# Optimization experiments

Measured on AMD Instinct MI355X. Metric: run time of the kernel, lower is better.

## Reference

```python
import jax, jax.numpy as jnp
import numpy as np

B, BITS, HID = 4096, 64, 512
EPS = 1e-5
TEMPERATURE = 1.0  # buffer default


def _w(k, shape):
    return jax.random.normal(k, shape, jnp.float32) * 0.02


def setup_inputs() -> dict:
    key = jax.random.key(0)
    ks = jax.random.split(key, 8)
    return {
        "a_bits": jax.random.uniform(ks[0], (B, BITS), jnp.float32),
        "shift_bits": jax.random.uniform(ks[1], (B, BITS), jnp.float32),
        # shift_decoder params
        "W1": _w(ks[2], (HID, BITS)), "b1": jnp.zeros((HID,), jnp.float32),
        "g1": jnp.ones((HID,), jnp.float32), "be1": jnp.zeros((HID,), jnp.float32),
        "W2": _w(ks[3], (HID, HID)), "b2": jnp.zeros((HID,), jnp.float32),
        "g2": jnp.ones((HID,), jnp.float32), "be2": jnp.zeros((HID,), jnp.float32),
        "W3": _w(ks[4], (BITS, HID)), "b3": jnp.zeros((BITS,), jnp.float32),
        # index_net params (input dim = 2*BITS)
        "Wi1": _w(ks[5], (HID, 2 * BITS)), "bi1": jnp.zeros((HID,), jnp.float32),
        "Wi2": _w(ks[6], (HID, HID)), "bi2": jnp.zeros((HID,), jnp.float32),
        "Wi3": _w(ks[7], (BITS, HID)), "bi3": jnp.zeros((BITS,), jnp.float32),
    }


def _layernorm(x, g, b):
    m = jnp.mean(x, axis=-1, keepdims=True)
    v = jnp.mean(jnp.square(x - m), axis=-1, keepdims=True)
    return (x - m) * jax.lax.rsqrt(v + EPS) * g + b


def reference(a_bits, shift_bits, W1, b1, g1, be1, W2, b2, g2, be2, W3, b3,
              Wi1, bi1, Wi2, bi2, Wi3, bi3):
    # shift decoder: Linear -> LN -> ReLU -> Linear -> LN -> ReLU -> Linear
    h = jax.nn.relu(_layernorm(shift_bits @ W1.T + b1, g1, be1))
    h = jax.nn.relu(_layernorm(h @ W2.T + b2, g2, be2))
    shift_logits = h @ W3.T + b3                        # [B, BITS]
    shift_soft = jax.nn.softmax(shift_logits / TEMPERATURE, axis=-1)

    # index_net, vectorized over the output-position loop.
    # combined = [one_hot(i), shift_soft]; the one-hot part of the first Linear
    # just selects column i of Wi1[:, :BITS], so we add it as a [BITS, HID] bias.
    pos_part = Wi1[:, :BITS].T                          # [BITS, HID]
    shift_part = shift_soft @ Wi1[:, BITS:].T           # [B, HID]
    h1 = jax.nn.relu(pos_part[None, :, :] + shift_part[:, None, :] + bi1)  # [B, BITS, HID]
    h2 = jax.nn.relu(jnp.einsum('bph,kh->bpk', h1, Wi2) + bi2)             # [B, BITS, HID]
    idx_logits = jnp.einsum('bph,kh->bpk', h2, Wi3) + bi3                  # [B, BITS, BITS]
    idx_soft = jax.nn.softmax(idx_logits / TEMPERATURE, axis=-1)

    # softmax-weighted gather-sum over a_bits
    return jnp.einsum('bpj,bj->bp', idx_soft, a_bits)   # [B, BITS]
```

## Files before the change

### kernel.cpp

```cpp
#include <hip/hip_runtime.h>
#include <hip/hip_bf16.h>
#include <math.h>

#define B_N 4096
#define BITSN 64
#define HID 512
#define EPSV 1e-5f
#define BT 16

typedef unsigned short ushort_t;
typedef __attribute__((ext_vector_type(8))) short bf16x8;
typedef __attribute__((ext_vector_type(4))) float f32x4;
typedef __attribute__((ext_vector_type(16))) float f32x16;

__device__ __forceinline__ ushort_t f2bf(float f) {
  unsigned u = __float_as_uint(f);
  u += 0x7FFF + ((u >> 16) & 1);
  return (ushort_t)(u >> 16);
}

__device__ __forceinline__ unsigned pack2bf(float lo, float hi) {
  union { __hip_bfloat162 h; unsigned u; } cv;
  cv.h = __float22bfloat162_rn(make_float2(lo, hi));
  return cv.u;
}

__device__ __forceinline__ float bf2f(short v) {
  return __uint_as_float(((unsigned)(unsigned short)v) << 16);
}

__global__ __launch_bounds__(256) void prep_kernel(
    const float* __restrict__ Wi2, const float* __restrict__ Wi3,
    const float* __restrict__ Wi1, const float* __restrict__ W1,
    const float* __restrict__ W2, const float* __restrict__ W3,
    ushort_t* __restrict__ Wi1posTb, ushort_t* __restrict__ W1b,
    ushort_t* __restrict__ W2f, ushort_t* __restrict__ W3b,
    ushort_t* __restrict__ Wi1sb, ushort_t* __restrict__ Wi2f32,
    ushort_t* __restrict__ Wi3g) {
  int idx = blockIdx.x * 256 + threadIdx.x;
  if (idx < 512 * 512) {
    {
      int j = idx & 7, lane = (idx >> 3) & 63;
      int ct = (idx >> 9) & 31, ks = idx >> 14;
      int c = ct * 16 + (lane & 15);
      int k = ks * 32 + (lane >> 4) * 8 + j;
      W2f[idx] = f2bf(W2[c * 512 + k]);
    }
    {
      int j = idx & 7, lane = (idx >> 3) & 63;
      int ct = (idx >> 9) & 15, ks = idx >> 13;
      int c = ct * 32 + (lane & 31);
      int k = ks * 16 + (lane >> 5) * 8 + j;
      Wi2f32[idx] = f2bf(Wi2[c * 512 + k]);
    }
  }
  if (idx < 64 * 512) {
    W3b[idx] = f2bf(W3[idx]);
    int p = idx >> 9, i = idx & 511;
    Wi1posTb[idx] = f2bf(Wi1[i * 128 + p]);
    int e = idx & 7, lane = (idx >> 3) & 63;
    int jt = (idx >> 9) & 1, h = (idx >> 10) & 1;
    int mc = (idx >> 11) & 1, w = idx >> 12;
    int jr = jt * 32 + (lane & 31);
    int c = w * 64 + mc * 32 + 16 * h + 4 * (lane >> 5) + (e & 3) + 8 * (e >> 2);
    Wi3g[idx] = f2bf(Wi3[jr * 512 + c]);
  }
  if (idx < 512 * 64) {
    W1b[idx] = f2bf(W1[idx]);
    int j = idx >> 6, k = idx & 63;
    Wi1sb[idx] = f2bf(Wi1[j * 128 + 64 + k]);
  }
}

__global__ __launch_bounds__(256) void shift2_kernel(
    const float* __restrict__ shift_bits,
    const ushort_t* __restrict__ W1b, const float* __restrict__ b1,
    const float* __restrict__ g1, const float* __restrict__ be1,
    const ushort_t* __restrict__ W2f, const float* __restrict__ b2,
    const float* __restrict__ g2, const float* __restrict__ be2,
    const ushort_t* __restrict__ W3b, const float* __restrict__ b3,
    const ushort_t* __restrict__ Wi1sb, const float* __restrict__ bi1,
    float* __restrict__ sp) {
  __shared__ __align__(16) ushort_t hA[BT * 512];
  __shared__ __align__(16) char reg2[32 * 1024];
  __shared__ float b1s[512], g1s[512], be1s[512];
  __shared__ float b2s[512], g2s[512], be2s[512], bi1s[512];
  __shared__ float red[4][BT][2];
  __shared__ float b3s[64];

  ushort_t* sbt = (ushort_t*)reg2;
  ushort_t* h2  = (ushort_t*)reg2;
  float (*lg32)[68] = (float(*)[68])(reg2 + 16 * 1024);
  ushort_t* sb2 = (ushort_t*)(reg2 + 16 * 1024 + 16 * 68 * 4);

  int b0 = blockIdx.x * BT;
  int t = threadIdx.x, w = t >> 6, l = t & 63, lg = l >> 4, l15 = l & 15;

  b1s[t] = b1[t];  b1s[t + 256] = b1[t + 256];
  g1s[t] = g1[t];  g1s[t + 256] = g1[t + 256];
  be1s[t] = be1[t]; be1s[t + 256] = be1[t + 256];
  b2s[t] = b2[t];  b2s[t + 256] = b2[t + 256];
  g2s[t] = g2[t];  g2s[t + 256] = g2[t + 256];
  be2s[t] = be2[t]; be2s[t + 256] = be2[t + 256];
  bi1s[t] = bi1[t]; bi1s[t + 256] = bi1[t + 256];
  if (t < 64) b3s[t] = b3[t];
  if (t < 128) {
    int row = t >> 3, g = t & 7;
    const float* src = shift_bits + (size_t)(b0 + row) * 64 + g * 8;
    uint4 pk;
    pk.x = (unsigned)f2bf(src[0]) | ((unsigned)f2bf(src[1]) << 16);
    pk.y = (unsigned)f2bf(src[2]) | ((unsigned)f2bf(src[3]) << 16);
    pk.z = (unsigned)f2bf(src[4]) | ((unsigned)f2bf(src[5]) << 16);
    pk.w = (unsigned)f2bf(src[6]) | ((unsigned)f2bf(src[7]) << 16);
    *(uint4*)((char*)sbt + ((row * 128 + g * 16) ^ ((row & 7) << 4))) = pk;
  }
  __syncthreads();

  f32x4 acc[8];
#pragma unroll
  for (int nt = 0; nt < 8; ++nt) acc[nt] = (f32x4){0.f, 0.f, 0.f, 0.f};
#pragma unroll
  for (int ks = 0; ks < 2; ++ks) {
    bf16x8 af = *(const bf16x8*)((char*)sbt + ((l15 * 128 + ks * 64 + lg * 16) ^ ((l15 & 7) << 4)));
#pragma unroll
    for (int nt = 0; nt < 8; ++nt) {
      int c = w * 128 + nt * 16 + l15;
      bf16x8 bfr = *(const bf16x8*)(W1b + (size_t)c * 64 + ks * 32 + lg * 8);
      acc[nt] = __builtin_amdgcn_mfma_f32_16x16x32_bf16(af, bfr, acc[nt], 0, 0, 0);
    }
  }
  {
    float s[4] = {0.f, 0.f, 0.f, 0.f}, q[4] = {0.f, 0.f, 0.f, 0.f};
#pragma unroll
    for (int nt = 0; nt < 8; ++nt) {
      int c = w * 128 + nt * 16 + l15;
      float bb = b1s[c];
#pragma unroll
      for (int r = 0; r < 4; ++r) {
        float x = acc[nt][r] + bb;
        acc[nt][r] = x;
        s[r] += x; q[r] += x * x;
      }
    }
#pragma unroll
    for (int m = 8; m >= 1; m >>= 1)
#pragma unroll
      for (int r = 0; r < 4; ++r) { s[r] += __shfl_xor(s[r], m); q[r] += __shfl_xor(q[r], m); }
    if (l15 == 0)
#pragma unroll
      for (int r = 0; r < 4; ++r) { red[w][4 * lg + r][0] = s[r]; red[w][4 * lg + r][1] = q[r]; }
    __syncthreads();
    float mean[4], rs[4];
#pragma unroll
    for (int r = 0; r < 4; ++r) {
      int p = 4 * lg + r;
      float S = red[0][p][0] + red[1][p][0] + red[2][p][0] + red[3][p][0];
      float Q = red[0][p][1] + red[1][p][1] + red[2][p][1] + red[3][p][1];
      mean[r] = S * (1.0f / 512.0f);
      float var = Q * (1.0f / 512.0f) - mean[r] * mean[r];
      rs[r] = rsqrtf(var + EPSV);
    }
#pragma unroll
    for (int nt = 0; nt < 8; ++nt) {
      int c = w * 128 + nt * 16 + l15;
      float gg = g1s[c], bb = be1s[c];
#pragma unroll
      for (int r = 0; r < 4; ++r) {
        int p = 4 * lg + r;
        float v = (acc[nt][r] - mean[r]) * rs[r] * gg + bb;
        v = v > 0.f ? v : 0.f;
        *(ushort_t*)((char*)hA + ((p * 1024 + c * 2) ^ ((p & 7) << 4))) = f2bf(v);
      }
    }
  }
  __syncthreads();

#pragma unroll
  for (int nt = 0; nt < 8; ++nt) acc[nt] = (f32x4){0.f, 0.f, 0.f, 0.f};
  {
    const bf16x8* w2base = (const bf16x8*)W2f + ((size_t)(w * 8) * 64 + l);
#pragma unroll 2
    for (int step = 0; step < 16; ++step) {
      bf16x8 af = *(const bf16x8*)((char*)hA + ((l15 * 1024 + step * 64 + lg * 16) ^ ((l15 & 7) << 4)));
#pragma unroll
      for (int nt = 0; nt < 8; ++nt) {
        bf16x8 bfr = w2base[((size_t)step * 32 + nt) * 64];
        acc[nt] = __builtin_amdgcn_mfma_f32_16x16x32_bf16(af, bfr, acc[nt], 0, 0, 0);
      }
    }
  }
  __syncthreads();
  {
    float s[4] = {0.f, 0.f, 0.f, 0.f}, q[4] = {0.f, 0.f, 0.f, 0.f};
#pragma unroll
    for (int nt = 0; nt < 8; ++nt) {
      int c = w * 128 + nt * 16 + l15;
      float bb = b2s[c];
#pragma unroll
      for (int r = 0; r < 4; ++r) {
        float x = acc[nt][r] + bb;
        acc[nt][r] = x;
        s[r] += x; q[r] += x * x;
      }
    }
#pragma unroll
    for (int m = 8; m >= 1; m >>= 1)
#pragma unroll
      for (int r = 0; r < 4; ++r) { s[r] += __shfl_xor(s[r], m); q[r] += __shfl_xor(q[r], m); }
    if (l15 == 0)
#pragma unroll
      for (int r = 0; r < 4; ++r) { red[w][4 * lg + r][0] = s[r]; red[w][4 * lg + r][1] = q[r]; }
    __syncthreads();
    float mean[4], rs[4];
#pragma unroll
    for (int r = 0; r < 4; ++r) {
      int p = 4 * lg + r;
      float S = red[0][p][0] + red[1][p][0] + red[2][p][0] + red[3][p][0];
      float Q = red[0][p][1] + red[1][p][1] + red[2][p][1] + red[3][p][1];
      mean[r] = S * (1.0f / 512.0f);
      float var = Q * (1.0f / 512.0f) - mean[r] * mean[r];
      rs[r] = rsqrtf(var + EPSV);
    }
#pragma unroll
    for (int nt = 0; nt < 8; ++nt) {
      int c = w * 128 + nt * 16 + l15;
      float gg = g2s[c], bb = be2s[c];
#pragma unroll
      for (int r = 0; r < 4; ++r) {
        int p = 4 * lg + r;
        float v = (acc[nt][r] - mean[r]) * rs[r] * gg + bb;
        v = v > 0.f ? v : 0.f;
        *(ushort_t*)((char*)h2 + ((p * 1024 + c * 2) ^ ((p & 7) << 4))) = f2bf(v);
      }
    }
  }
  __syncthreads();

  {
    f32x4 a3 = (f32x4){0.f, 0.f, 0.f, 0.f};
#pragma unroll
    for (int ks = 0; ks < 16; ++ks) {
      bf16x8 af = *(const bf16x8*)((char*)h2 + ((l15 * 1024 + ks * 64 + lg * 16) ^ ((l15 & 7) << 4)));
      bf16x8 bfr = *(const bf16x8*)(W3b + (size_t)(w * 16 + l15) * 512 + ks * 32 + lg * 8);
      a3 = __builtin_amdgcn_mfma_f32_16x16x32_bf16(af, bfr, a3, 0, 0, 0);
    }
    int c = w * 16 + l15;
    float bb = b3s[c];
#pragma unroll
    for (int r = 0; r < 4; ++r) lg32[4 * lg + r][c] = a3[r] + bb;
  }
  __syncthreads();

  {
    int r = t >> 4, j = t & 15;
    float v[4];
    float m = -1e30f;
#pragma unroll
    for (int mq = 0; mq < 4; ++mq) { v[mq] = lg32[r][mq * 16 + j]; m = fmaxf(m, v[mq]); }
#pragma unroll
    for (int mk = 8; mk >= 1; mk >>= 1) m = fmaxf(m, __shfl_xor(m, mk));
    float ssum = 0.f;
#pragma unroll
    for (int mq = 0; mq < 4; ++mq) { v[mq] = expf(v[mq] - m); ssum += v[mq]; }
#pragma unroll
    for (int mk = 8; mk >= 1; mk >>= 1) ssum += __shfl_xor(ssum, mk);
    float inv = 1.f / ssum;
#pragma unroll
    for (int mq = 0; mq < 4; ++mq) {
      int c = mq * 16 + j;
      *(ushort_t*)((char*)sb2 + ((r * 128 + c * 2) ^ ((r & 7) << 4))) = f2bf(v[mq] * inv);
    }
  }
  __syncthreads();

  {
    f32x4 a4[8];
#pragma unroll
    for (int nt = 0; nt < 8; ++nt) a4[nt] = (f32x4){0.f, 0.f, 0.f, 0.f};
#pragma unroll
    for (int ks = 0; ks < 2; ++ks) {
      bf16x8 af = *(const bf16x8*)((char*)sb2 + ((l15 * 128 + ks * 64 + lg * 16) ^ ((l15 & 7) << 4)));
#pragma unroll
      for (int nt = 0; nt < 8; ++nt) {
        int c = w * 128 + nt * 16 + l15;
        bf16x8 bfr = *(const bf16x8*)(Wi1sb + (size_t)c * 64 + ks * 32 + lg * 8);
        a4[nt] = __builtin_amdgcn_mfma_f32_16x16x32_bf16(af, bfr, a4[nt], 0, 0, 0);
      }
    }
#pragma unroll
    for (int nt = 0; nt < 8; ++nt) {
      int c = w * 128 + nt * 16 + l15;
      float bb = bi1s[c];
#pragma unroll
      for (int r = 0; r < 4; ++r)
        sp[(size_t)(b0 + 4 * lg + r) * 512 + c] = a4[nt][r] + bb;
    }
  }
}

__global__ __launch_bounds__(512, 4) void big9_kernel(
    const float* __restrict__ a_bits, const float* __restrict__ sp,
    const ushort_t* __restrict__ posTb,
    const ushort_t* __restrict__ Wi2f32, const ushort_t* __restrict__ Wi3g,
    const float* __restrict__ bi2, const float* __restrict__ bi3,
    float* __restrict__ out) {
  __shared__ __align__(16) ushort_t h1s[64 * 512];
  __shared__ float bi2s[512];
  __shared__ float ab[64];
  __shared__ float bi3s[64];

  int b = blockIdx.x, t = threadIdx.x;
  int w = t >> 6, l = t & 63;
  int l31 = l & 31, hi = l >> 5;

  bi2s[t] = bi2[t];
  if (t < 64) { ab[t] = a_bits[b * 64 + t]; bi3s[t] = bi3[t]; }

  {
    const float* sprow = sp + (size_t)b * 512 + l * 8;
    float4 s0 = *(const float4*)(sprow);
    float4 s1 = *(const float4*)(sprow + 4);
#pragma unroll
    for (int g = 0; g < 8; ++g) {
      int p = g * 8 + w;
      bf16x8 pr = *(const bf16x8*)(posTb + (size_t)p * 512 + l * 8);
      float v0 = fmaxf(s0.x + bf2f(pr[0]), 0.f), v1 = fmaxf(s0.y + bf2f(pr[1]), 0.f);
      float v2 = fmaxf(s0.z + bf2f(pr[2]), 0.f), v3 = fmaxf(s0.w + bf2f(pr[3]), 0.f);
      float v4 = fmaxf(s1.x + bf2f(pr[4]), 0.f), v5 = fmaxf(s1.y + bf2f(pr[5]), 0.f);
      float v6 = fmaxf(s1.z + bf2f(pr[6]), 0.f), v7 = fmaxf(s1.w + bf2f(pr[7]), 0.f);
      uint4 pk;
      pk.x = pack2bf(v0, v1); pk.y = pack2bf(v2, v3);
      pk.z = pack2bf(v4, v5); pk.w = pack2bf(v6, v7);
      *(uint4*)((char*)h1s + ((p * 1024 + l * 16) ^ ((p & 15) << 4))) = pk;
    }
  }
  __syncthreads();

  f32x16 acc[2][2];
#pragma unroll
  for (int mc = 0; mc < 2; ++mc)
#pragma unroll
    for (int np = 0; np < 2; ++np)
#pragma unroll
      for (int r = 0; r < 16; ++r) acc[mc][np][r] = 0.f;

  {
    const bf16x8* bbase = (const bf16x8*)Wi2f32 + ((size_t)(2 * w) * 64 + l);
    bf16x8 wf[4][2];
#pragma unroll
    for (int d = 0; d < 4; ++d) {
      wf[d][0] = bbase[(size_t)d * 1024];
      wf[d][1] = bbase[(size_t)d * 1024 + 64];
    }
    for (int kb = 0; kb < 8; ++kb) {
#pragma unroll
      for (int d = 0; d < 4; ++d) {
        int ks = kb * 4 + d;
        bf16x8 w0 = wf[d][0], w1 = wf[d][1];
        if (kb < 7) {
          wf[d][0] = bbase[(size_t)(ks + 4) * 1024];
          wf[d][1] = bbase[(size_t)(ks + 4) * 1024 + 64];
        }
        int row0 = l31, row1 = 32 + l31;
        bf16x8 h0 = *(const bf16x8*)((char*)h1s + ((row0 * 1024 + ks * 32 + hi * 16) ^ ((row0 & 15) << 4)));
        bf16x8 h1v = *(const bf16x8*)((char*)h1s + ((row1 * 1024 + ks * 32 + hi * 16) ^ ((row1 & 15) << 4)));
        __builtin_amdgcn_s_setprio(1);
        acc[0][0] = __builtin_amdgcn_mfma_f32_32x32x16_bf16(w0, h0, acc[0][0], 0, 0, 0);
        acc[0][1] = __builtin_amdgcn_mfma_f32_32x32x16_bf16(w0, h1v, acc[0][1], 0, 0, 0);
        acc[1][0] = __builtin_amdgcn_mfma_f32_32x32x16_bf16(w1, h0, acc[1][0], 0, 0, 0);
        acc[1][1] = __builtin_amdgcn_mfma_f32_32x32x16_bf16(w1, h1v, acc[1][1], 0, 0, 0);
        __builtin_amdgcn_s_setprio(0);
      }
    }
  }

  bf16x8 pkf[2][2][2];
#pragma unroll
  for (int mc = 0; mc < 2; ++mc) {
    float bia[16];
#pragma unroll
    for (int rq = 0; rq < 4; ++rq) {
      int c0 = w * 64 + mc * 32 + 8 * rq + 4 * hi;
      float4 bi4 = *(const float4*)(bi2s + c0);
      bia[4 * rq + 0] = bi4.x; bia[4 * rq + 1] = bi4.y;
      bia[4 * rq + 2] = bi4.z; bia[4 * rq + 3] = bi4.w;
    }
#pragma unroll
    for (int np = 0; np < 2; ++np) {
      float hv[16];
#pragma unroll
      for (int r = 0; r < 16; ++r) hv[r] = fmaxf(acc[mc][np][r] + bia[r], 0.f);
#pragma unroll
      for (int h = 0; h < 2; ++h) {
        unsigned d0 = pack2bf(hv[8 * h + 0], hv[8 * h + 1]);
        unsigned d1 = pack2bf(hv[8 * h + 2], hv[8 * h + 3]);
        unsigned d2 = pack2bf(hv[8 * h + 4], hv[8 * h + 5]);
        unsigned d3 = pack2bf(hv[8 * h + 6], hv[8 * h + 7]);
        union { unsigned u[4]; bf16x8 v; } cv;
        cv.u[0] = d0; cv.u[1] = d1; cv.u[2] = d2; cv.u[3] = d3;
        pkf[np][mc][h] = cv.v;
      }
    }
  }
  __syncthreads();

  f32x16 l00, l01, l10, l11;
#pragma unroll
  for (int r = 0; r < 16; ++r) { l00[r] = 0.f; l01[r] = 0.f; l10[r] = 0.f; l11[r] = 0.f; }
  {
    const bf16x8* gbase = (const bf16x8*)Wi3g + ((size_t)w * 8 * 64 + l);
#pragma unroll
    for (int mc = 0; mc < 2; ++mc) {
#pragma unroll
      for (int h = 0; h < 2; ++h) {
        bf16x8 g0 = gbase[((mc * 2 + h) * 2 + 0) * 64];
        bf16x8 g1 = gbase[((mc * 2 + h) * 2 + 1) * 64];
        __builtin_amdgcn_s_setprio(1);
        l00 = __builtin_amdgcn_mfma_f32_32x32x16_bf16(pkf[0][mc][h], g0, l00, 0, 0, 0);
        l01 = __builtin_amdgcn_mfma_f32_32x32x16_bf16(pkf[0][mc][h], g1, l01, 0, 0, 0);
        l10 = __builtin_amdgcn_mfma_f32_32x32x16_bf16(pkf[1][mc][h], g0, l10, 0, 0, 0);
        l11 = __builtin_amdgcn_mfma_f32_32x32x16_bf16(pkf[1][mc][h], g1, l11, 0, 0, 0);
        __builtin_amdgcn_s_setprio(0);
      }
    }
  }

  {
    ushort_t* Pr = h1s + (size_t)w * 4096;
#pragma unroll
    for (int r = 0; r < 16; ++r) {
      int p0 = (r & 3) + 8 * (r >> 2) + 4 * hi;
      int p1 = p0 + 32;
      Pr[p0 * 64 + ((l31)      ^ (8 * (p0 & 7)))] = f2bf(l00[r]);
      Pr[p0 * 64 + ((32 + l31) ^ (8 * (p0 & 7)))] = f2bf(l01[r]);
      Pr[p1 * 64 + ((l31)      ^ (8 * (p1 & 7)))] = f2bf(l10[r]);
      Pr[p1 * 64 + ((32 + l31) ^ (8 * (p1 & 7)))] = f2bf(l11[r]);
    }
  }
  __syncthreads();

  {
    int p = t >> 3, jo = t & 7;
    int off = p * 64 + ((jo ^ (p & 7)) * 8);
    float sum[8] = {0.f, 0.f, 0.f, 0.f, 0.f, 0.f, 0.f, 0.f};
#pragma unroll
    for (int wr = 0; wr < 8; ++wr) {
      bf16x8 v = *(const bf16x8*)(h1s + wr * 4096 + off);
#pragma unroll
      for (int m = 0; m < 8; ++m) sum[m] += bf2f(v[m]);
    }
    float s = 0.f, g = 0.f;
#pragma unroll
    for (int m = 0; m < 8; ++m) {
      int c = jo * 8 + m;
      float e = __expf(sum[m] + bi3s[c]);
      s += e; g += e * ab[c];
    }
#pragma unroll
    for (int mm = 4; mm >= 1; mm >>= 1) { s += __shfl_xor(s, mm); g += __shfl_xor(g, mm); }
    if (jo == 0) out[b * 64 + p] = g / s;
  }
}

extern "C" void kernel_launch(void* const* d_in, const int* in_sizes, int n_in,
                              void* d_out, int out_size, void* d_ws, size_t ws_size,
                              hipStream_t stream) {
  const float* a_bits     = (const float*)d_in[0];
  const float* shift_bits = (const float*)d_in[1];
  const float* W1  = (const float*)d_in[2];
  const float* b1  = (const float*)d_in[3];
  const float* g1  = (const float*)d_in[4];
  const float* be1 = (const float*)d_in[5];
  const float* W2  = (const float*)d_in[6];
  const float* b2  = (const float*)d_in[7];
  const float* g2  = (const float*)d_in[8];
  const float* be2 = (const float*)d_in[9];
  const float* W3  = (const float*)d_in[10];
  const float* b3  = (const float*)d_in[11];
  const float* Wi1 = (const float*)d_in[12];
  const float* bi1 = (const float*)d_in[13];
  const float* Wi2 = (const float*)d_in[14];
  const float* bi2 = (const float*)d_in[15];
  const float* Wi3 = (const float*)d_in[16];
  const float* bi3 = (const float*)d_in[17];
  float* out = (float*)d_out;

  float* sp = (float*)d_ws;
  ushort_t* W2f = (ushort_t*)((char*)d_ws + (size_t)B_N * HID * 4);
  ushort_t* W1b = W2f + 512 * 512;
  ushort_t* W3b = W1b + 512 * 64;
  ushort_t* Wi1sb = W3b + 64 * 512;
  ushort_t* Wi1posTb = Wi1sb + 512 * 64;
  ushort_t* Wi2f32 = Wi1posTb + 64 * 512;
  ushort_t* Wi3g = Wi2f32 + 512 * 512;

  prep_kernel<<<1024, 256, 0, stream>>>(Wi2, Wi3, Wi1, W1, W2, W3,
                                        Wi1posTb, W1b, W2f, W3b, Wi1sb, Wi2f32, Wi3g);
  shift2_kernel<<<B_N / BT, 256, 0, stream>>>(shift_bits, W1b, b1, g1, be1,
                                              W2f, b2, g2, be2, W3b, b3, Wi1sb, bi1, sp);
  big9_kernel<<<B_N, 512, 0, stream>>>(a_bits, sp, Wi1posTb, Wi2f32, Wi3g, bi2, bi3, out);
}
```

Measured before the change: 202.2 us.

## Stage h2 in LDS and compute final layer without cross-wave K-split reduction

Before, each wave computed partial index logits over its own 64-column slice of h2 using register-held fragments. Those bf16 partials were written to LDS and summed across 8 waves before the softmax. Now each wave writes its ReLU'd h2 tile into LDS (reusing the swizzled h1 buffer). Each wave then computes a full-K 16x32 block of logits with 16x16x32 MFMAs and writes fp32 logits to a padded LDS array for the softmax-gather. This removes the 8-way partial-sum pass and the bf16 rounding of partials, at the cost of an extra LDS round trip for h2 and more barriers.

New measurement: 202.2 us. Within noise of the previous version (-0.0%).

```diff
diff --git a/kernel.cpp b/kernel.cpp
--- a/kernel.cpp
+++ b/kernel.cpp
@@ -36,7 +36,7 @@
     ushort_t* __restrict__ Wi1posTb, ushort_t* __restrict__ W1b,
     ushort_t* __restrict__ W2f, ushort_t* __restrict__ W3b,
     ushort_t* __restrict__ Wi1sb, ushort_t* __restrict__ Wi2f32,
-    ushort_t* __restrict__ Wi3g) {
+    ushort_t* __restrict__ Wi3f) {
   int idx = blockIdx.x * 256 + threadIdx.x;
   if (idx < 512 * 512) {
     {
@@ -58,12 +58,11 @@
     W3b[idx] = f2bf(W3[idx]);
     int p = idx >> 9, i = idx & 511;
     Wi1posTb[idx] = f2bf(Wi1[i * 128 + p]);
-    int e = idx & 7, lane = (idx >> 3) & 63;
-    int jt = (idx >> 9) & 1, h = (idx >> 10) & 1;
-    int mc = (idx >> 11) & 1, w = idx >> 12;
-    int jr = jt * 32 + (lane & 31);
-    int c = w * 64 + mc * 32 + 16 * h + 4 * (lane >> 5) + (e & 3) + 8 * (e >> 2);
-    Wi3g[idx] = f2bf(Wi3[jr * 512 + c]);
+    int j = idx & 7, lane = (idx >> 3) & 63;
+    int nt = (idx >> 9) & 3, ks2 = idx >> 11;
+    int jr = nt * 16 + (lane & 15);
+    int k = ks2 * 32 + (lane >> 4) * 8 + j;
+    Wi3f[idx] = f2bf(Wi3[jr * 512 + k]);
   }
   if (idx < 512 * 64) {
     W1b[idx] = f2bf(W1[idx]);
@@ -298,10 +297,10 @@
   }
 }
 
-__global__ __launch_bounds__(512, 4) void big9_kernel(
+__global__ __launch_bounds__(512, 4) void big10_kernel(
     const float* __restrict__ a_bits, const float* __restrict__ sp,
     const ushort_t* __restrict__ posTb,
-    const ushort_t* __restrict__ Wi2f32, const ushort_t* __restrict__ Wi3g,
+    const ushort_t* __restrict__ Wi2f32, const ushort_t* __restrict__ Wi3f,
     const float* __restrict__ bi2, const float* __restrict__ bi3,
     float* __restrict__ out) {
   __shared__ __align__(16) ushort_t h1s[64 * 512];
@@ -312,6 +311,7 @@
   int b = blockIdx.x, t = threadIdx.x;
   int w = t >> 6, l = t & 63;
   int l31 = l & 31, hi = l >> 5;
+  int lg = l >> 4, l15 = l & 15;
 
   bi2s[t] = bi2[t];
   if (t < 64) { ab[t] = a_bits[b * 64 + t]; bi3s[t] = bi3[t]; }
@@ -373,87 +373,73 @@
       }
     }
   }
-
-  bf16x8 pkf[2][2][2];
+  __syncthreads();
+
 #pragma unroll
   for (int mc = 0; mc < 2; ++mc) {
-    float bia[16];
-#pragma unroll
-    for (int rq = 0; rq < 4; ++rq) {
-      int c0 = w * 64 + mc * 32 + 8 * rq + 4 * hi;
-      float4 bi4 = *(const float4*)(bi2s + c0);
-      bia[4 * rq + 0] = bi4.x; bia[4 * rq + 1] = bi4.y;
-      bia[4 * rq + 2] = bi4.z; bia[4 * rq + 3] = bi4.w;
-    }
 #pragma unroll
     for (int np = 0; np < 2; ++np) {
-      float hv[16];
-#pragma unroll
-      for (int r = 0; r < 16; ++r) hv[r] = fmaxf(acc[mc][np][r] + bia[r], 0.f);
-#pragma unroll
-      for (int h = 0; h < 2; ++h) {
-        unsigned d0 = pack2bf(hv[8 * h + 0], hv[8 * h + 1]);
-        unsigned d1 = pack2bf(hv[8 * h + 2], hv[8 * h + 3]);
-        unsigned d2 = pack2bf(hv[8 * h + 4], hv[8 * h + 5]);
-        unsigned d3 = pack2bf(hv[8 * h + 6], hv[8 * h + 7]);
-        union { unsigned u[4]; bf16x8 v; } cv;
-        cv.u[0] = d0; cv.u[1] = d1; cv.u[2] = d2; cv.u[3] = d3;
-        pkf[np][mc][h] = cv.v;
-      }
-    }
-  }
-  __syncthreads();
-
-  f32x16 l00, l01, l10, l11;
-#pragma unroll
-  for (int r = 0; r < 16; ++r) { l00[r] = 0.f; l01[r] = 0.f; l10[r] = 0.f; l11[r] = 0.f; }
-  {
-    const bf16x8* gbase = (const bf16x8*)Wi3g + ((size_t)w * 8 * 64 + l);
-#pragma unroll
-    for (int mc = 0; mc < 2; ++mc) {
-#pragma unroll
-      for (int h = 0; h < 2; ++h) {
-        bf16x8 g0 = gbase[((mc * 2 + h) * 2 + 0) * 64];
-        bf16x8 g1 = gbase[((mc * 2 + h) * 2 + 1) * 64];
-        __builtin_amdgcn_s_setprio(1);
-        l00 = __builtin_amdgcn_mfma_f32_32x32x16_bf16(pkf[0][mc][h], g0, l00, 0, 0, 0);
-        l01 = __builtin_amdgcn_mfma_f32_32x32x16_bf16(pkf[0][mc][h], g1, l01, 0, 0, 0);
-        l10 = __builtin_amdgcn_mfma_f32_32x32x16_bf16(pkf[1][mc][h], g0, l10, 0, 0, 0);
-        l11 = __builtin_amdgcn_mfma_f32_32x32x16_bf16(pkf[1][mc][h], g1, l11, 0, 0, 0);
-        __builtin_amdgcn_s_setprio(0);
-      }
-    }
-  }
-
-  {
-    ushort_t* Pr = h1s + (size_t)w * 4096;
-#pragma unroll
-    for (int r = 0; r < 16; ++r) {
-      int p0 = (r & 3) + 8 * (r >> 2) + 4 * hi;
-      int p1 = p0 + 32;
-      Pr[p0 * 64 + ((l31)      ^ (8 * (p0 & 7)))] = f2bf(l00[r]);
-      Pr[p0 * 64 + ((32 + l31) ^ (8 * (p0 & 7)))] = f2bf(l01[r]);
-      Pr[p1 * 64 + ((l31)      ^ (8 * (p1 & 7)))] = f2bf(l10[r]);
-      Pr[p1 * 64 + ((32 + l31) ^ (8 * (p1 & 7)))] = f2bf(l11[r]);
-    }
-  }
-  __syncthreads();
-
-  {
+      int p = np * 32 + l31;
+#pragma unroll
+      for (int rq = 0; rq < 4; ++rq) {
+        int c0 = w * 64 + mc * 32 + 8 * rq + 4 * hi;
+        float4 bi4 = *(const float4*)(bi2s + c0);
+        float v0 = fmaxf(acc[mc][np][4 * rq + 0] + bi4.x, 0.f);
+        float v1 = fmaxf(acc[mc][np][4 * rq + 1] + bi4.y, 0.f);
+        float v2 = fmaxf(acc[mc][np][4 * rq + 2] + bi4.z, 0.f);
+        float v3 = fmaxf(acc[mc][np][4 * rq + 3] + bi4.w, 0.f);
+        uint2 pk;
+        pk.x = pack2bf(v0, v1);
+        pk.y = pack2bf(v2, v3);
+        *(uint2*)((char*)h1s + ((p * 1024 + c0 * 2) ^ ((p & 15) << 4))) = pk;
+      }
+    }
+  }
+  __syncthreads();
+
+  f32x4 lacc[2];
+  lacc[0] = (f32x4){0.f, 0.f, 0.f, 0.f};
+  lacc[1] = (f32x4){0.f, 0.f, 0.f, 0.f};
+  {
+    int pw = w >> 1, jh = w & 1;
+    int p2 = 16 * pw + l15;
+    const bf16x8* b3base = (const bf16x8*)Wi3f + l;
+#pragma unroll 4
+    for (int ks2 = 0; ks2 < 16; ++ks2) {
+      bf16x8 a2 = *(const bf16x8*)((char*)h1s + ((p2 * 1024 + ks2 * 64 + lg * 16) ^ ((p2 & 15) << 4)));
+      bf16x8 g0 = b3base[(ks2 * 4 + 2 * jh + 0) * 64];
+      bf16x8 g1 = b3base[(ks2 * 4 + 2 * jh + 1) * 64];
+      __builtin_amdgcn_s_setprio(1);
+      lacc[0] = __builtin_amdgcn_mfma_f32_16x16x32_bf16(a2, g0, lacc[0], 0, 0, 0);
+      lacc[1] = __builtin_amdgcn_mfma_f32_16x16x32_bf16(a2, g1, lacc[1], 0, 0, 0);
+      __builtin_amdgcn_s_setprio(0);
+    }
+  }
+  __syncthreads();
+
+  {
+    float* Lg = (float*)h1s;
+    int pw = w >> 1, jh = w & 1;
+#pragma unroll
+    for (int q = 0; q < 2; ++q) {
+      int j = (2 * jh + q) * 16 + l15;
+#pragma unroll
+      for (int r = 0; r < 4; ++r) {
+        int p = pw * 16 + 4 * lg + r;
+        Lg[p * 68 + j] = lacc[q][r];
+      }
+    }
+  }
+  __syncthreads();
+
+  {
+    const float* Lg = (const float*)h1s;
     int p = t >> 3, jo = t & 7;
-    int off = p * 64 + ((jo ^ (p & 7)) * 8);
-    float sum[8] = {0.f, 0.f, 0.f, 0.f, 0.f, 0.f, 0.f, 0.f};
-#pragma unroll
-    for (int wr = 0; wr < 8; ++wr) {
-      bf16x8 v = *(const bf16x8*)(h1s + wr * 4096 + off);
-#pragma unroll
-      for (int m = 0; m < 8; ++m) sum[m] += bf2f(v[m]);
-    }
     float s = 0.f, g = 0.f;
 #pragma unroll
     for (int m = 0; m < 8; ++m) {
       int c = jo * 8 + m;
-      float e = __expf(sum[m] + bi3s[c]);
+      float e = __expf(Lg[p * 68 + c] + bi3s[c]);
       s += e; g += e * ab[c];
     }
 #pragma unroll
@@ -492,11 +478,11 @@
   ushort_t* Wi1sb = W3b + 64 * 512;
   ushort_t* Wi1posTb = Wi1sb + 512 * 64;
   ushort_t* Wi2f32 = Wi1posTb + 64 * 512;
-  ushort_t* Wi3g = Wi2f32 + 512 * 512;
+  ushort_t* Wi3f = Wi2f32 + 512 * 512;
 
   prep_kernel<<<1024, 256, 0, stream>>>(Wi2, Wi3, Wi1, W1, W2, W3,
-                                        Wi1posTb, W1b, W2f, W3b, Wi1sb, Wi2f32, Wi3g);
+                                        Wi1posTb, W1b, W2f, W3b, Wi1sb, Wi2f32, Wi3f);
   shift2_kernel<<<B_N / BT, 256, 0, stream>>>(shift_bits, W1b, b1, g1, be1,
                                               W2f, b2, g2, be2, W3b, b3, Wi1sb, bi1, sp);
-  big9_kernel<<<B_N, 512, 0, stream>>>(a_bits, sp, Wi1posTb, Wi2f32, Wi3g, bi2, bi3, out);
-}
+  big10_kernel<<<B_N, 512, 0, stream>>>(a_bits, sp, Wi1posTb, Wi2f32, Wi3f, bi2, bi3, out);
+}
```
